# Kernel optimization log

Measured on AMD Instinct MI355X. Metric: run time of the kernel, lower is better.

## Reference

```python
import jax, jax.numpy as jnp
import numpy as np
import math

N_NODES = 50000
N_EDGES = 400000
D = 256
H = 4
HD = D // H


def _layernorm(x, g, b, eps=1e-5):
    mu = jnp.mean(x, axis=-1, keepdims=True)
    var = jnp.mean((x - mu) ** 2, axis=-1, keepdims=True)
    return (x - mu) * jax.lax.rsqrt(var + eps) * g + b


def setup_inputs() -> dict:
    key = jax.random.key(0)
    ks = jax.random.split(key, 16)
    init = lambda k, sh: (jax.random.normal(k, sh, dtype=jnp.float32) * 0.02)
    inp = {
        "h_n": jax.random.normal(ks[0], (N_NODES, D), dtype=jnp.float32),
        "h_e": jax.random.normal(ks[1], (N_EDGES, D), dtype=jnp.float32),
        "edge_index": jax.random.randint(ks[2], (2, N_EDGES), 0, N_NODES, dtype=jnp.int64),
        "Wq_w": init(ks[3], (2 * D, D)), "Wq_b": jnp.zeros((D,), jnp.float32),
        "Wkv_w": init(ks[4], (2 * D, 2 * D)), "Wkv_b": jnp.zeros((2 * D,), jnp.float32),
        "Wo_w": init(ks[5], (D, D)), "Wo_b": jnp.zeros((D,), jnp.float32),
        "ln1_g": jnp.ones((D,), jnp.float32), "ln1_b": jnp.zeros((D,), jnp.float32),
        "ffn1_w": init(ks[6], (D, 4 * D)), "ffn1_b": jnp.zeros((4 * D,), jnp.float32),
        "ffn2_w": init(ks[7], (4 * D, D)), "ffn2_b": jnp.zeros((D,), jnp.float32),
        "ln2_g": jnp.ones((D,), jnp.float32), "ln2_b": jnp.zeros((D,), jnp.float32),
    }
    return inp


def reference(h_n, h_e, edge_index, Wq_w, Wq_b, Wkv_w, Wkv_b, Wo_w, Wo_b,
              ln1_g, ln1_b, ffn1_w, ffn1_b, ffn2_w, ffn2_b, ln2_g, ln2_b):
    num_nodes = h_n.shape[0]
    src, dst = edge_index[0], edge_index[1]

    # edge gathers
    q_input = jnp.concatenate([h_n[src], h_e], axis=-1)   # (E, 2D)
    kv_input = jnp.concatenate([h_n[dst], h_e], axis=-1)  # (E, 2D)

    Q = q_input @ Wq_w + Wq_b                             # (E, D)
    KV = kv_input @ Wkv_w + Wkv_b                         # (E, 2D)
    K, V = KV[:, :D], KV[:, D:]

    Q = Q.reshape(-1, H, HD)
    K = K.reshape(-1, H, HD)
    V = V.reshape(-1, H, HD)

    scores = jnp.sum(Q * K, axis=-1) / math.sqrt(HD)      # (E, H)

    # scatter softmax over edges grouped by src node
    m = jax.ops.segment_max(scores, src, num_segments=num_nodes)  # (N, H)
    ex = jnp.exp(scores - m[src])
    denom = jax.ops.segment_sum(ex, src, num_segments=num_nodes)  # (N, H)
    attn = ex / denom[src]                                        # (E, H)

    # scatter-sum of weighted values back to src nodes
    wv = attn[:, :, None] * V                                     # (E, H, HD)
    out = jax.ops.segment_sum(wv, src, num_segments=num_nodes)    # (N, H, HD)
    out = out.reshape(num_nodes, D)
    out = out @ Wo_w + Wo_b

    h = _layernorm(h_n + out, ln1_g, ln1_b)
    ff = jax.nn.gelu(h @ ffn1_w + ffn1_b, approximate=False) @ ffn2_w + ffn2_b
    h = _layernorm(h + ff, ln2_g, ln2_b)
    return h
```

## Files before the change

kernel.cpp:

```cpp
#include <hip/hip_runtime.h>
#include <hip/hip_bf16.h>
#include <cstdint>
#include <cstddef>


typedef __bf16 bf16;
typedef bf16 bf16x8 __attribute__((ext_vector_type(8)));
typedef bf16 bf16x4v __attribute__((ext_vector_type(4)));
typedef float f32x4 __attribute__((ext_vector_type(4)));
typedef const uint32_t __attribute__((address_space(1)))* gas_u32p;
typedef uint32_t __attribute__((address_space(3)))* las_u32p;

#define DEV static __device__ __forceinline__

static constexpr int NN = 50000;
static constexpr int NE = 400000;

DEV void async_copy16(const void* g, void* l) {
  __builtin_amdgcn_global_load_lds((gas_u32p)g, (las_u32p)l, 16, 0, 0);
}
DEV float bf2f(bf16 x) { return (float)x; }
DEV bf16  f2bf(float x) { return (bf16)x; }

template <int KV>
__global__ __launch_bounds__(256, 2) void gemm_edge(
    const bf16* __restrict__ hn, const bf16* __restrict__ he,
    const int* __restrict__ idx, const bf16* __restrict__ WT,
    const float* __restrict__ bias, const bf16* __restrict__ Qbf,
    bf16* __restrict__ outbf, float* __restrict__ scores) {
  __shared__ bf16 Al[128 * 32];
  __shared__ bf16 Bl[128 * 32];
  const int tid = threadIdx.x;
  const int e0 = blockIdx.x * 128;
  const int n0 = blockIdx.y * 128;

  const bf16* an[2];
  const bf16* ae[2];
  const bf16* bb[2];
#pragma unroll
  for (int p = 0; p < 2; ++p) {
    int c = tid + 256 * p;
    int row = c >> 2;
    int c8 = (c & 3) * 8;
    int e = e0 + row;
    int node = idx[e];
    an[p] = hn + (size_t)node * 256 + c8;
    ae[p] = he + (size_t)e * 256 + c8;
    bb[p] = WT + (size_t)(n0 + row) * 512 + c8;
  }

  const int wv = tid >> 6, lane = tid & 63;
  const int quad = lane >> 4, l16 = lane & 15;
  const int wrow = (wv >> 1) * 64, wcol = (wv & 1) * 64;

  f32x4 acc[4][4] = {};

  for (int k0 = 0; k0 < 512; k0 += 32) {
    if (k0) __syncthreads();
#pragma unroll
    for (int p = 0; p < 2; ++p) {
      const bf16* ga = (k0 < 256) ? (an[p] + k0) : (ae[p] + (k0 - 256));
      async_copy16(ga, &Al[(tid + 256 * p) * 8]);
      async_copy16(bb[p] + k0, &Bl[(tid + 256 * p) * 8]);
    }
    __syncthreads();
    bf16x8 af[4], bfr[4];
#pragma unroll
    for (int t = 0; t < 4; ++t)
      af[t] = *(const bf16x8*)&Al[(wrow + t * 16 + l16) * 32 + quad * 8];
#pragma unroll
    for (int t = 0; t < 4; ++t)
      bfr[t] = *(const bf16x8*)&Bl[(wcol + t * 16 + l16) * 32 + quad * 8];
#pragma unroll
    for (int mt = 0; mt < 4; ++mt)
#pragma unroll
      for (int nt = 0; nt < 4; ++nt)
        acc[mt][nt] = __builtin_amdgcn_mfma_f32_16x16x32_bf16(
            af[mt], bfr[nt], acc[mt][nt], 0, 0, 0);
  }

  if (KV == 0) {
#pragma unroll
    for (int nt = 0; nt < 4; ++nt) {
      int col = n0 + wcol + nt * 16 + l16;
      float bv = bias[col];
#pragma unroll
      for (int mt = 0; mt < 4; ++mt)
#pragma unroll
        for (int r = 0; r < 4; ++r) {
          int row = e0 + wrow + mt * 16 + quad * 4 + r;
          outbf[(size_t)row * 256 + col] = f2bf(acc[mt][nt][r] + bv);
        }
    }
  } else if (blockIdx.y < 2) {
    const int head = (n0 + wcol) >> 6;
    float bv[4];
#pragma unroll
    for (int nt = 0; nt < 4; ++nt) bv[nt] = bias[n0 + wcol + nt * 16 + l16];
#pragma unroll
    for (int mt = 0; mt < 4; ++mt)
#pragma unroll
      for (int r = 0; r < 4; ++r) {
        int row = e0 + wrow + mt * 16 + quad * 4 + r;
        float part = 0.f;
#pragma unroll
        for (int nt = 0; nt < 4; ++nt) {
          int col = n0 + wcol + nt * 16 + l16;
          part += (acc[mt][nt][r] + bv[nt]) * bf2f(Qbf[(size_t)row * 256 + col]);
        }
        part += __shfl_xor(part, 1);
        part += __shfl_xor(part, 2);
        part += __shfl_xor(part, 4);
        part += __shfl_xor(part, 8);
        if (l16 == 0) scores[(size_t)row * 4 + head] = part * 0.125f;
      }
  } else {
#pragma unroll
    for (int nt = 0; nt < 4; ++nt) {
      int col = n0 + wcol + nt * 16 + l16;
      float bv = bias[col];
#pragma unroll
      for (int mt = 0; mt < 4; ++mt)
#pragma unroll
        for (int r = 0; r < 4; ++r) {
          int row = e0 + wrow + mt * 16 + quad * 4 + r;
          outbf[(size_t)row * 256 + (col - 256)] = f2bf(acc[mt][nt][r] + bv);
        }
    }
  }
}

template <int KT, int EPI>
__global__ __launch_bounds__(256, 2) void gemm_node(
    const bf16* __restrict__ A, int M, const bf16* __restrict__ WT,
    const float* __restrict__ bias, int Nout, float* __restrict__ outf,
    bf16* __restrict__ outb) {
  __shared__ bf16 Al[128 * 32];
  __shared__ bf16 Bl[128 * 32];
  const int tid = threadIdx.x;
  const int m0 = blockIdx.x * 128;
  const int n0 = blockIdx.y * 128;
  const bf16* ab[2];
  const bf16* bb[2];
#pragma unroll
  for (int p = 0; p < 2; ++p) {
    int c = tid + 256 * p;
    int row = c >> 2;
    int c8 = (c & 3) * 8;
    int rg = m0 + row;
    if (rg > M - 1) rg = M - 1;
    ab[p] = A + (size_t)rg * KT + c8;
    bb[p] = WT + (size_t)(n0 + row) * KT + c8;
  }
  const int wv = tid >> 6, lane = tid & 63;
  const int quad = lane >> 4, l16 = lane & 15;
  const int wrow = (wv >> 1) * 64, wcol = (wv & 1) * 64;
  f32x4 acc[4][4] = {};
  for (int k0 = 0; k0 < KT; k0 += 32) {
    if (k0) __syncthreads();
#pragma unroll
    for (int p = 0; p < 2; ++p) {
      async_copy16(ab[p] + k0, &Al[(tid + 256 * p) * 8]);
      async_copy16(bb[p] + k0, &Bl[(tid + 256 * p) * 8]);
    }
    __syncthreads();
    bf16x8 af[4], bfr[4];
#pragma unroll
    for (int t = 0; t < 4; ++t)
      af[t] = *(const bf16x8*)&Al[(wrow + t * 16 + l16) * 32 + quad * 8];
#pragma unroll
    for (int t = 0; t < 4; ++t)
      bfr[t] = *(const bf16x8*)&Bl[(wcol + t * 16 + l16) * 32 + quad * 8];
#pragma unroll
    for (int mt = 0; mt < 4; ++mt)
#pragma unroll
      for (int nt = 0; nt < 4; ++nt)
        acc[mt][nt] = __builtin_amdgcn_mfma_f32_16x16x32_bf16(
            af[mt], bfr[nt], acc[mt][nt], 0, 0, 0);
  }
#pragma unroll
  for (int nt = 0; nt < 4; ++nt) {
    int col = n0 + wcol + nt * 16 + l16;
    float bv = bias[col];
#pragma unroll
    for (int mt = 0; mt < 4; ++mt)
#pragma unroll
      for (int r = 0; r < 4; ++r) {
        int row = m0 + wrow + mt * 16 + quad * 4 + r;
        if (row < M) {
          float v = acc[mt][nt][r] + bv;
          if (EPI == 0)
            outf[(size_t)row * Nout + col] = v;
          else
            outb[(size_t)row * Nout + col] =
                f2bf(0.5f * v * (1.f + erff(v * 0.70710678118654752f)));
        }
      }
  }
}

__global__ __launch_bounds__(256) void cast_bf16(const float* __restrict__ in,
                                                 bf16* __restrict__ out, int n) {
  int i = (blockIdx.x * 256 + threadIdx.x) * 4;
  if (i < n) {
    float4 v = *(const float4*)(in + i);
    bf16x4v o = {f2bf(v.x), f2bf(v.y), f2bf(v.z), f2bf(v.w)};
    *(bf16x4v*)(out + i) = o;
  }
}

__global__ __launch_bounds__(256) void transpose_cast(
    const float* __restrict__ W, bf16* __restrict__ WT, int K, int N) {
  int i = blockIdx.x * 256 + threadIdx.x;
  if (i < K * N) {
    int k = i / N, n = i - k * N;
    WT[(size_t)n * K + k] = f2bf(W[i]);
  }
}

__global__ __launch_bounds__(256) void count_deg(const int* __restrict__ src,
                                                 int* __restrict__ deg, int nE) {
  int e = blockIdx.x * 256 + threadIdx.x;
  if (e < nE) atomicAdd(&deg[src[e]], 1);
}

__global__ __launch_bounds__(256) void scan_offs(const int* __restrict__ deg,
                                                 int* __restrict__ offs,
                                                 int* __restrict__ cursor,
                                                 int nN) {
  __shared__ int part[256];
  int tid = threadIdx.x;
  int per = (nN + 255) >> 8;
  int lo = tid * per, hi = lo + per;
  if (hi > nN) hi = nN;
  int sm = 0;
  for (int i = lo; i < hi; ++i) sm += deg[i];
  part[tid] = sm;
  __syncthreads();
  if (tid == 0) {
    int run = 0;
    for (int i = 0; i < 256; ++i) {
      int v = part[i];
      part[i] = run;
      run += v;
    }
  }
  __syncthreads();
  int run = part[tid];
  for (int i = lo; i < hi; ++i) {
    offs[i] = run;
    cursor[i] = run;
    run += deg[i];
  }
  if (tid == 255) offs[nN] = run;
}

__global__ __launch_bounds__(256) void scatter_edges(const int* __restrict__ src,
                                                     int* __restrict__ cursor,
                                                     int* __restrict__ eperm,
                                                     int nE) {
  int e = blockIdx.x * 256 + threadIdx.x;
  if (e < nE) {
    int p = atomicAdd(&cursor[src[e]], 1);
    eperm[p] = e;
  }
}

__global__ __launch_bounds__(256) void aggregate(
    const int* __restrict__ offs, const int* __restrict__ eperm,
    const float* __restrict__ scores, const bf16* __restrict__ Vbf,
    bf16* __restrict__ outbf) {
  int n = blockIdx.x;
  int s = offs[n];
  int deg = offs[n + 1] - s;
  int tid = threadIdx.x, wv = tid >> 6, lane = tid & 63;
  __shared__ float mdl[4], dnl[4];
  float mx = -3.4e38f;
  for (int i = lane; i < deg; i += 64) {
    int e = eperm[s + i];
    mx = fmaxf(mx, scores[(size_t)e * 4 + wv]);
  }
#pragma unroll
  for (int o = 32; o; o >>= 1) mx = fmaxf(mx, __shfl_xor(mx, o));
  float sm = 0.f;
  for (int i = lane; i < deg; i += 64) {
    int e = eperm[s + i];
    sm += expf(scores[(size_t)e * 4 + wv] - mx);
  }
#pragma unroll
  for (int o = 32; o; o >>= 1) sm += __shfl_xor(sm, o);
  if (lane == 0) {
    mdl[wv] = mx;
    dnl[wv] = sm;
  }
  __syncthreads();
  int c = tid, h = tid >> 6;
  float m = mdl[h];
  float rd = dnl[h] > 0.f ? 1.f / dnl[h] : 0.f;
  float acc = 0.f;
  for (int i = 0; i < deg; ++i) {
    int e = eperm[s + i];
    float w = expf(scores[(size_t)e * 4 + h] - m) * rd;
    acc += w * bf2f(Vbf[(size_t)e * 256 + c]);
  }
  outbf[(size_t)n * 256 + c] = f2bf(acc);
}

__global__ __launch_bounds__(256) void ln_kernel(
    const float* __restrict__ x1, const float* __restrict__ x2,
    const float* __restrict__ g, const float* __restrict__ b,
    float* __restrict__ outf, bf16* __restrict__ outb) {
  int n = blockIdx.x, tid = threadIdx.x;
  float x = x1[(size_t)n * 256 + tid] + x2[(size_t)n * 256 + tid];
  float s = x, s2 = x * x;
#pragma unroll
  for (int o = 32; o; o >>= 1) {
    s += __shfl_xor(s, o);
    s2 += __shfl_xor(s2, o);
  }
  __shared__ float ls[4], ls2[4];
  int wv = tid >> 6, lane = tid & 63;
  if (lane == 0) {
    ls[wv] = s;
    ls2[wv] = s2;
  }
  __syncthreads();
  s = ls[0] + ls[1] + ls[2] + ls[3];
  s2 = ls2[0] + ls2[1] + ls2[2] + ls2[3];
  float mu = s * (1.f / 256.f);
  float var = s2 * (1.f / 256.f) - mu * mu;
  float y = (x - mu) * rsqrtf(var + 1e-5f) * g[tid] + b[tid];
  if (outf) outf[(size_t)n * 256 + tid] = y;
  if (outb) outb[(size_t)n * 256 + tid] = f2bf(y);
}

static constexpr size_t OFF_HN = 0;
static constexpr size_t OFF_HE = OFF_HN + 25600000;
static constexpr size_t OFF_WQT = OFF_HE + 204800000;
static constexpr size_t OFF_WKVT = OFF_WQT + 262144;
static constexpr size_t OFF_WOT = OFF_WKVT + 524288;
static constexpr size_t OFF_W1T = OFF_WOT + 131072;
static constexpr size_t OFF_W2T = OFF_W1T + 524288;
static constexpr size_t OFF_SC = OFF_W2T + 524288;
static constexpr size_t OFF_DEG = OFF_SC + 6400000;
static constexpr size_t OFF_OFFS = OFF_DEG + 200000;
static constexpr size_t OFF_CUR = OFF_OFFS + 200064;
static constexpr size_t OFF_EPERM = OFF_CUR + 200000;
static constexpr size_t OFF_AOUT = OFF_EPERM + 1600000;
static constexpr size_t OFF_Q = OFF_AOUT + 25600000;
static constexpr size_t OFF_V = OFF_Q + 204800000;
static constexpr size_t OFF_TMP = OFF_Q;
static constexpr size_t OFF_H1F = OFF_Q + 51200000;
static constexpr size_t OFF_H1B = OFF_Q + 102400000;
static constexpr size_t OFF_TMP2 = OFF_Q + 128000000;
static constexpr size_t OFF_FFM = OFF_HE;

extern "C" void kernel_launch(void* const* d_in, const int* in_sizes, int n_in,
                              void* d_out, int out_size, void* d_ws,
                              size_t ws_size, hipStream_t stream) {
  const float* h_n = (const float*)d_in[0];
  const float* h_e = (const float*)d_in[1];
  const int* eidx = (const int*)d_in[2];
  const int* src = eidx;
  const int* dst = eidx + NE;
  const float* Wq_w = (const float*)d_in[3];
  const float* Wq_b = (const float*)d_in[4];
  const float* Wkv_w = (const float*)d_in[5];
  const float* Wkv_b = (const float*)d_in[6];
  const float* Wo_w = (const float*)d_in[7];
  const float* Wo_b = (const float*)d_in[8];
  const float* ln1_g = (const float*)d_in[9];
  const float* ln1_b = (const float*)d_in[10];
  const float* f1_w = (const float*)d_in[11];
  const float* f1_b = (const float*)d_in[12];
  const float* f2_w = (const float*)d_in[13];
  const float* f2_b = (const float*)d_in[14];
  const float* ln2_g = (const float*)d_in[15];
  const float* ln2_b = (const float*)d_in[16];

  uint8_t* ws = (uint8_t*)d_ws;
  bf16* hn_bf = (bf16*)(ws + OFF_HN);
  bf16* he_bf = (bf16*)(ws + OFF_HE);
  bf16* WqT = (bf16*)(ws + OFF_WQT);
  bf16* WkvT = (bf16*)(ws + OFF_WKVT);
  bf16* WoT = (bf16*)(ws + OFF_WOT);
  bf16* W1T = (bf16*)(ws + OFF_W1T);
  bf16* W2T = (bf16*)(ws + OFF_W2T);
  float* scores = (float*)(ws + OFF_SC);
  int* deg = (int*)(ws + OFF_DEG);
  int* offs = (int*)(ws + OFF_OFFS);
  int* cursor = (int*)(ws + OFF_CUR);
  int* eperm = (int*)(ws + OFF_EPERM);
  bf16* aout = (bf16*)(ws + OFF_AOUT);
  bf16* Qbf = (bf16*)(ws + OFF_Q);
  bf16* Vbf = (bf16*)(ws + OFF_V);
  float* tmp = (float*)(ws + OFF_TMP);
  float* h1f = (float*)(ws + OFF_H1F);
  bf16* h1b = (bf16*)(ws + OFF_H1B);
  float* tmp2 = (float*)(ws + OFF_TMP2);
  bf16* ffm = (bf16*)(ws + OFF_FFM);

  cast_bf16<<<12500, 256, 0, stream>>>(h_n, hn_bf, NN * 256);
  cast_bf16<<<100000, 256, 0, stream>>>(h_e, he_bf, NE * 256);
  transpose_cast<<<512, 256, 0, stream>>>(Wq_w, WqT, 512, 256);
  transpose_cast<<<1024, 256, 0, stream>>>(Wkv_w, WkvT, 512, 512);
  transpose_cast<<<256, 256, 0, stream>>>(Wo_w, WoT, 256, 256);
  transpose_cast<<<1024, 256, 0, stream>>>(f1_w, W1T, 256, 1024);
  transpose_cast<<<1024, 256, 0, stream>>>(f2_w, W2T, 1024, 256);

  hipMemsetAsync(deg, 0, NN * sizeof(int), stream);
  count_deg<<<1563, 256, 0, stream>>>(src, deg, NE);
  scan_offs<<<1, 256, 0, stream>>>(deg, offs, cursor, NN);
  scatter_edges<<<1563, 256, 0, stream>>>(src, cursor, eperm, NE);

  gemm_edge<0><<<dim3(3125, 2), 256, 0, stream>>>(hn_bf, he_bf, src, WqT, Wq_b,
                                                  nullptr, Qbf, nullptr);
  gemm_edge<1><<<dim3(3125, 4), 256, 0, stream>>>(hn_bf, he_bf, dst, WkvT,
                                                  Wkv_b, Qbf, Vbf, scores);

  aggregate<<<NN, 256, 0, stream>>>(offs, eperm, scores, Vbf, aout);

  gemm_node<256, 0><<<dim3(391, 2), 256, 0, stream>>>(aout, NN, WoT, Wo_b, 256,
                                                      tmp, nullptr);
  ln_kernel<<<NN, 256, 0, stream>>>(h_n, tmp, ln1_g, ln1_b, h1f, h1b);

  gemm_node<256, 1><<<dim3(391, 8), 256, 0, stream>>>(h1b, NN, W1T, f1_b, 1024,
                                                      nullptr, ffm);
  gemm_node<1024, 0><<<dim3(391, 2), 256, 0, stream>>>(ffm, NN, W2T, f2_b, 256,
                                                       tmp2, nullptr);
  ln_kernel<<<NN, 256, 0, stream>>>(h1f, tmp2, ln2_g, ln2_b, (float*)d_out,
                                    nullptr);
}
```

Baseline: 1.893 ms.

## Split node/edge projections and fold V projection into output weight

Uses linearity to project node features once per node (50k rows) instead of per gathered edge, and adds the gathered node projection in the edge GEMM epilogues. The V projection is eliminated by aggregating raw hn[dst] and he rows per head and multiplying by a precomputed Wkv_V·Wo combined weight (K=2048) at node level. This cuts edge-level GEMM FLOPs and V writes, but adds fp32 node-projection gathers, a per-head 2048-wide aggregated buffer, and a larger node GEMM. Grid axes are also swapped so N-tiles vary fastest.

```diff
diff --git a/kernel.cpp b/kernel.cpp
--- a/kernel.cpp
+++ b/kernel.cpp
@@ -21,114 +21,6 @@
 }
 DEV float bf2f(bf16 x) { return (float)x; }
 DEV bf16  f2bf(float x) { return (bf16)x; }
-
-template <int KV>
-__global__ __launch_bounds__(256, 2) void gemm_edge(
-    const bf16* __restrict__ hn, const bf16* __restrict__ he,
-    const int* __restrict__ idx, const bf16* __restrict__ WT,
-    const float* __restrict__ bias, const bf16* __restrict__ Qbf,
-    bf16* __restrict__ outbf, float* __restrict__ scores) {
-  __shared__ bf16 Al[128 * 32];
-  __shared__ bf16 Bl[128 * 32];
-  const int tid = threadIdx.x;
-  const int e0 = blockIdx.x * 128;
-  const int n0 = blockIdx.y * 128;
-
-  const bf16* an[2];
-  const bf16* ae[2];
-  const bf16* bb[2];
-#pragma unroll
-  for (int p = 0; p < 2; ++p) {
-    int c = tid + 256 * p;
-    int row = c >> 2;
-    int c8 = (c & 3) * 8;
-    int e = e0 + row;
-    int node = idx[e];
-    an[p] = hn + (size_t)node * 256 + c8;
-    ae[p] = he + (size_t)e * 256 + c8;
-    bb[p] = WT + (size_t)(n0 + row) * 512 + c8;
-  }
-
-  const int wv = tid >> 6, lane = tid & 63;
-  const int quad = lane >> 4, l16 = lane & 15;
-  const int wrow = (wv >> 1) * 64, wcol = (wv & 1) * 64;
-
-  f32x4 acc[4][4] = {};
-
-  for (int k0 = 0; k0 < 512; k0 += 32) {
-    if (k0) __syncthreads();
-#pragma unroll
-    for (int p = 0; p < 2; ++p) {
-      const bf16* ga = (k0 < 256) ? (an[p] + k0) : (ae[p] + (k0 - 256));
-      async_copy16(ga, &Al[(tid + 256 * p) * 8]);
-      async_copy16(bb[p] + k0, &Bl[(tid + 256 * p) * 8]);
-    }
-    __syncthreads();
-    bf16x8 af[4], bfr[4];
-#pragma unroll
-    for (int t = 0; t < 4; ++t)
-      af[t] = *(const bf16x8*)&Al[(wrow + t * 16 + l16) * 32 + quad * 8];
-#pragma unroll
-    for (int t = 0; t < 4; ++t)
-      bfr[t] = *(const bf16x8*)&Bl[(wcol + t * 16 + l16) * 32 + quad * 8];
-#pragma unroll
-    for (int mt = 0; mt < 4; ++mt)
-#pragma unroll
-      for (int nt = 0; nt < 4; ++nt)
-        acc[mt][nt] = __builtin_amdgcn_mfma_f32_16x16x32_bf16(
-            af[mt], bfr[nt], acc[mt][nt], 0, 0, 0);
-  }
-
-  if (KV == 0) {
-#pragma unroll
-    for (int nt = 0; nt < 4; ++nt) {
-      int col = n0 + wcol + nt * 16 + l16;
-      float bv = bias[col];
-#pragma unroll
-      for (int mt = 0; mt < 4; ++mt)
-#pragma unroll
-        for (int r = 0; r < 4; ++r) {
-          int row = e0 + wrow + mt * 16 + quad * 4 + r;
-          outbf[(size_t)row * 256 + col] = f2bf(acc[mt][nt][r] + bv);
-        }
-    }
-  } else if (blockIdx.y < 2) {
-    const int head = (n0 + wcol) >> 6;
-    float bv[4];
-#pragma unroll
-    for (int nt = 0; nt < 4; ++nt) bv[nt] = bias[n0 + wcol + nt * 16 + l16];
-#pragma unroll
-    for (int mt = 0; mt < 4; ++mt)
-#pragma unroll
-      for (int r = 0; r < 4; ++r) {
-        int row = e0 + wrow + mt * 16 + quad * 4 + r;
-        float part = 0.f;
-#pragma unroll
-        for (int nt = 0; nt < 4; ++nt) {
-          int col = n0 + wcol + nt * 16 + l16;
-          part += (acc[mt][nt][r] + bv[nt]) * bf2f(Qbf[(size_t)row * 256 + col]);
-        }
-        part += __shfl_xor(part, 1);
-        part += __shfl_xor(part, 2);
-        part += __shfl_xor(part, 4);
-        part += __shfl_xor(part, 8);
-        if (l16 == 0) scores[(size_t)row * 4 + head] = part * 0.125f;
-      }
-  } else {
-#pragma unroll
-    for (int nt = 0; nt < 4; ++nt) {
-      int col = n0 + wcol + nt * 16 + l16;
-      float bv = bias[col];
-#pragma unroll
-      for (int mt = 0; mt < 4; ++mt)
-#pragma unroll
-        for (int r = 0; r < 4; ++r) {
-          int row = e0 + wrow + mt * 16 + quad * 4 + r;
-          outbf[(size_t)row * 256 + (col - 256)] = f2bf(acc[mt][nt][r] + bv);
-        }
-    }
-  }
-}
 
 template <int KT, int EPI>
 __global__ __launch_bounds__(256, 2) void gemm_node(
@@ -138,8 +30,8 @@
   __shared__ bf16 Al[128 * 32];
   __shared__ bf16 Bl[128 * 32];
   const int tid = threadIdx.x;
-  const int m0 = blockIdx.x * 128;
-  const int n0 = blockIdx.y * 128;
+  const int n0 = blockIdx.x * 128;
+  const int m0 = blockIdx.y * 128;
   const bf16* ab[2];
   const bf16* bb[2];
 #pragma unroll
@@ -181,7 +73,7 @@
 #pragma unroll
   for (int nt = 0; nt < 4; ++nt) {
     int col = n0 + wcol + nt * 16 + l16;
-    float bv = bias[col];
+    float bv = bias ? bias[col] : 0.f;
 #pragma unroll
     for (int mt = 0; mt < 4; ++mt)
 #pragma unroll
@@ -191,12 +83,150 @@
           float v = acc[mt][nt][r] + bv;
           if (EPI == 0)
             outf[(size_t)row * Nout + col] = v;
-          else
+          else if (EPI == 1)
             outb[(size_t)row * Nout + col] =
                 f2bf(0.5f * v * (1.f + erff(v * 0.70710678118654752f)));
+          else
+            outb[(size_t)row * Nout + col] = f2bf(v);
         }
       }
   }
+}
+
+__global__ __launch_bounds__(256, 2) void gemm_eeq(
+    const bf16* __restrict__ he, const bf16* __restrict__ WT,
+    const float* __restrict__ bias, const int* __restrict__ src,
+    const float* __restrict__ ENf, bf16* __restrict__ Qout) {
+  __shared__ bf16 Al[128 * 32];
+  __shared__ bf16 Bl[128 * 32];
+  const int tid = threadIdx.x;
+  const int n0 = blockIdx.x * 128;
+  const int m0 = blockIdx.y * 128;
+  const bf16* ab[2];
+  const bf16* bb[2];
+#pragma unroll
+  for (int p = 0; p < 2; ++p) {
+    int c = tid + 256 * p;
+    int row = c >> 2;
+    int c8 = (c & 3) * 8;
+    ab[p] = he + (size_t)(m0 + row) * 256 + c8;
+    bb[p] = WT + (size_t)(n0 + row) * 256 + c8;
+  }
+  const int wv = tid >> 6, lane = tid & 63;
+  const int quad = lane >> 4, l16 = lane & 15;
+  const int wrow = (wv >> 1) * 64, wcol = (wv & 1) * 64;
+  f32x4 acc[4][4] = {};
+  for (int k0 = 0; k0 < 256; k0 += 32) {
+    if (k0) __syncthreads();
+#pragma unroll
+    for (int p = 0; p < 2; ++p) {
+      async_copy16(ab[p] + k0, &Al[(tid + 256 * p) * 8]);
+      async_copy16(bb[p] + k0, &Bl[(tid + 256 * p) * 8]);
+    }
+    __syncthreads();
+    bf16x8 af[4], bfr[4];
+#pragma unroll
+    for (int t = 0; t < 4; ++t)
+      af[t] = *(const bf16x8*)&Al[(wrow + t * 16 + l16) * 32 + quad * 8];
+#pragma unroll
+    for (int t = 0; t < 4; ++t)
+      bfr[t] = *(const bf16x8*)&Bl[(wcol + t * 16 + l16) * 32 + quad * 8];
+#pragma unroll
+    for (int mt = 0; mt < 4; ++mt)
+#pragma unroll
+      for (int nt = 0; nt < 4; ++nt)
+        acc[mt][nt] = __builtin_amdgcn_mfma_f32_16x16x32_bf16(
+            af[mt], bfr[nt], acc[mt][nt], 0, 0, 0);
+  }
+  float bv[4];
+#pragma unroll
+  for (int nt = 0; nt < 4; ++nt) bv[nt] = bias[n0 + wcol + nt * 16 + l16];
+#pragma unroll
+  for (int mt = 0; mt < 4; ++mt)
+#pragma unroll
+    for (int r = 0; r < 4; ++r) {
+      int row = m0 + wrow + mt * 16 + quad * 4 + r;
+      int s = src[row];
+      const float* en = ENf + (size_t)s * 512;
+#pragma unroll
+      for (int nt = 0; nt < 4; ++nt) {
+        int col = n0 + wcol + nt * 16 + l16;
+        Qout[(size_t)row * 256 + col] = f2bf(acc[mt][nt][r] + bv[nt] + en[col]);
+      }
+    }
+}
+
+__global__ __launch_bounds__(256, 2) void gemm_eek(
+    const bf16* __restrict__ he, const bf16* __restrict__ WT,
+    const float* __restrict__ bias, const int* __restrict__ dstp,
+    const float* __restrict__ ENf, const bf16* __restrict__ Qbf,
+    float* __restrict__ scores) {
+  __shared__ bf16 Al[128 * 32];
+  __shared__ bf16 Bl[128 * 32];
+  const int tid = threadIdx.x;
+  const int n0 = blockIdx.x * 128;
+  const int m0 = blockIdx.y * 128;
+  const bf16* ab[2];
+  const bf16* bb[2];
+#pragma unroll
+  for (int p = 0; p < 2; ++p) {
+    int c = tid + 256 * p;
+    int row = c >> 2;
+    int c8 = (c & 3) * 8;
+    ab[p] = he + (size_t)(m0 + row) * 256 + c8;
+    bb[p] = WT + (size_t)(n0 + row) * 256 + c8;
+  }
+  const int wv = tid >> 6, lane = tid & 63;
+  const int quad = lane >> 4, l16 = lane & 15;
+  const int wrow = (wv >> 1) * 64, wcol = (wv & 1) * 64;
+  f32x4 acc[4][4] = {};
+  for (int k0 = 0; k0 < 256; k0 += 32) {
+    if (k0) __syncthreads();
+#pragma unroll
+    for (int p = 0; p < 2; ++p) {
+      async_copy16(ab[p] + k0, &Al[(tid + 256 * p) * 8]);
+      async_copy16(bb[p] + k0, &Bl[(tid + 256 * p) * 8]);
+    }
+    __syncthreads();
+    bf16x8 af[4], bfr[4];
+#pragma unroll
+    for (int t = 0; t < 4; ++t)
+      af[t] = *(const bf16x8*)&Al[(wrow + t * 16 + l16) * 32 + quad * 8];
+#pragma unroll
+    for (int t = 0; t < 4; ++t)
+      bfr[t] = *(const bf16x8*)&Bl[(wcol + t * 16 + l16) * 32 + quad * 8];
+#pragma unroll
+    for (int mt = 0; mt < 4; ++mt)
+#pragma unroll
+      for (int nt = 0; nt < 4; ++nt)
+        acc[mt][nt] = __builtin_amdgcn_mfma_f32_16x16x32_bf16(
+            af[mt], bfr[nt], acc[mt][nt], 0, 0, 0);
+  }
+  float bv[4];
+#pragma unroll
+  for (int nt = 0; nt < 4; ++nt) bv[nt] = bias[n0 + wcol + nt * 16 + l16];
+  const int head = (n0 + wcol) >> 6;
+#pragma unroll
+  for (int mt = 0; mt < 4; ++mt)
+#pragma unroll
+    for (int r = 0; r < 4; ++r) {
+      int row = m0 + wrow + mt * 16 + quad * 4 + r;
+      int d = dstp[row];
+      const float* en = ENf + (size_t)d * 512 + 256;
+      const bf16* qr = Qbf + (size_t)row * 256;
+      float part = 0.f;
+#pragma unroll
+      for (int nt = 0; nt < 4; ++nt) {
+        int col = n0 + wcol + nt * 16 + l16;
+        float kv = acc[mt][nt][r] + bv[nt] + en[col];
+        part += kv * bf2f(qr[col]);
+      }
+      part += __shfl_xor(part, 1);
+      part += __shfl_xor(part, 2);
+      part += __shfl_xor(part, 4);
+      part += __shfl_xor(part, 8);
+      if (l16 == 0) scores[(size_t)row * 4 + head] = part * 0.125f;
+    }
 }
 
 __global__ __launch_bounds__(256) void cast_bf16(const float* __restrict__ in,
@@ -216,6 +246,51 @@
     int k = i / N, n = i - k * N;
     WT[(size_t)n * K + k] = f2bf(W[i]);
   }
+}
+
+__global__ __launch_bounds__(256) void build_wnet(
+    const float* __restrict__ Wq, const float* __restrict__ Wkv,
+    bf16* __restrict__ WnT, bf16* __restrict__ WeT) {
+  int n = blockIdx.x, k = threadIdx.x;
+  float vn, ve;
+  if (n < 256) {
+    vn = Wq[(size_t)k * 256 + n];
+    ve = Wq[(size_t)(256 + k) * 256 + n];
+  } else {
+    vn = Wkv[(size_t)k * 512 + (n - 256)];
+    ve = Wkv[(size_t)(256 + k) * 512 + (n - 256)];
+  }
+  WnT[(size_t)n * 256 + k] = f2bf(vn);
+  WeT[(size_t)n * 256 + k] = f2bf(ve);
+}
+
+__global__ __launch_bounds__(256) void build_wcomb(
+    const float* __restrict__ Wkv, const float* __restrict__ Wkv_b,
+    const float* __restrict__ Wo, const float* __restrict__ Wo_b,
+    bf16* __restrict__ WcombT, float* __restrict__ bias_vo) {
+  int j = blockIdx.x, t = threadIdx.x;
+  __shared__ float wo[256];
+  wo[t] = Wo[(size_t)t * 256 + j];
+  __syncthreads();
+#pragma unroll
+  for (int p = 0; p < 8; ++p) {
+    int idx = p * 256 + t;
+    int h = idx >> 9, i = idx & 511;
+    const float* wrow = Wkv + (size_t)i * 512 + 256 + h * 64;
+    const float* wob = wo + h * 64;
+    float s = 0.f;
+#pragma unroll 8
+    for (int m = 0; m < 64; ++m) s += wrow[m] * wob[m];
+    WcombT[(size_t)j * 2048 + idx] = f2bf(s);
+  }
+  float bs = Wkv_b[256 + t] * wo[t];
+#pragma unroll
+  for (int o = 32; o; o >>= 1) bs += __shfl_xor(bs, o);
+  __shared__ float red[4];
+  int wv = t >> 6, lane = t & 63;
+  if (lane == 0) red[wv] = bs;
+  __syncthreads();
+  if (t == 0) bias_vo[j] = red[0] + red[1] + red[2] + red[3] + Wo_b[j];
 }
 
 __global__ __launch_bounds__(256) void count_deg(const int* __restrict__ src,
@@ -268,8 +343,9 @@
 
 __global__ __launch_bounds__(256) void aggregate(
     const int* __restrict__ offs, const int* __restrict__ eperm,
-    const float* __restrict__ scores, const bf16* __restrict__ Vbf,
-    bf16* __restrict__ outbf) {
+    const int* __restrict__ dstp, const float* __restrict__ scores,
+    const bf16* __restrict__ hn, const bf16* __restrict__ he,
+    bf16* __restrict__ aggH) {
   int n = blockIdx.x;
   int s = offs[n];
   int deg = offs[n + 1] - s;
@@ -294,16 +370,34 @@
     dnl[wv] = sm;
   }
   __syncthreads();
-  int c = tid, h = tid >> 6;
-  float m = mdl[h];
-  float rd = dnl[h] > 0.f ? 1.f / dnl[h] : 0.f;
-  float acc = 0.f;
+  float m[4], rd[4];
+#pragma unroll
+  for (int h = 0; h < 4; ++h) {
+    m[h] = mdl[h];
+    rd[h] = dnl[h] > 0.f ? 1.f / dnl[h] : 0.f;
+  }
+  float accn[4] = {}, acce[4] = {};
   for (int i = 0; i < deg; ++i) {
     int e = eperm[s + i];
-    float w = expf(scores[(size_t)e * 4 + h] - m) * rd;
-    acc += w * bf2f(Vbf[(size_t)e * 256 + c]);
-  }
-  outbf[(size_t)n * 256 + c] = f2bf(acc);
+    int d = dstp[e];
+    f32x4 sc = *(const f32x4*)(scores + (size_t)e * 4);
+    float w[4];
+#pragma unroll
+    for (int h = 0; h < 4; ++h) w[h] = expf(sc[h] - m[h]) * rd[h];
+    float xn = bf2f(hn[(size_t)d * 256 + tid]);
+    float xe = bf2f(he[(size_t)e * 256 + tid]);
+#pragma unroll
+    for (int h = 0; h < 4; ++h) {
+      accn[h] += w[h] * xn;
+      acce[h] += w[h] * xe;
+    }
+  }
+  bf16* out = aggH + (size_t)n * 2048;
+#pragma unroll
+  for (int h = 0; h < 4; ++h) {
+    out[h * 512 + tid] = f2bf(accn[h]);
+    out[h * 512 + 256 + tid] = f2bf(acce[h]);
+  }
 }
 
 __global__ __launch_bounds__(256) void ln_kernel(
@@ -334,26 +428,27 @@
   if (outb) outb[(size_t)n * 256 + tid] = f2bf(y);
 }
 
-static constexpr size_t OFF_HN = 0;
-static constexpr size_t OFF_HE = OFF_HN + 25600000;
-static constexpr size_t OFF_WQT = OFF_HE + 204800000;
-static constexpr size_t OFF_WKVT = OFF_WQT + 262144;
-static constexpr size_t OFF_WOT = OFF_WKVT + 524288;
-static constexpr size_t OFF_W1T = OFF_WOT + 131072;
-static constexpr size_t OFF_W2T = OFF_W1T + 524288;
-static constexpr size_t OFF_SC = OFF_W2T + 524288;
-static constexpr size_t OFF_DEG = OFF_SC + 6400000;
-static constexpr size_t OFF_OFFS = OFF_DEG + 200000;
-static constexpr size_t OFF_CUR = OFF_OFFS + 200064;
-static constexpr size_t OFF_EPERM = OFF_CUR + 200000;
-static constexpr size_t OFF_AOUT = OFF_EPERM + 1600000;
-static constexpr size_t OFF_Q = OFF_AOUT + 25600000;
-static constexpr size_t OFF_V = OFF_Q + 204800000;
-static constexpr size_t OFF_TMP = OFF_Q;
-static constexpr size_t OFF_H1F = OFF_Q + 51200000;
-static constexpr size_t OFF_H1B = OFF_Q + 102400000;
-static constexpr size_t OFF_TMP2 = OFF_Q + 128000000;
-static constexpr size_t OFF_FFM = OFF_HE;
+static constexpr size_t OFF_HN    = 0;
+static constexpr size_t OFF_HE    = 25600000;
+static constexpr size_t OFF_WNT   = 230400000;
+static constexpr size_t OFF_WET   = 230662144;
+static constexpr size_t OFF_WCT   = 230924288;
+static constexpr size_t OFF_W1T   = 231972864;
+static constexpr size_t OFF_W2T   = 232497152;
+static constexpr size_t OFF_BVO   = 233021440;
+static constexpr size_t OFF_SC    = 233022464;
+static constexpr size_t OFF_DEG   = 239422464;
+static constexpr size_t OFF_OFFS  = 239622464;
+static constexpr size_t OFF_CUR   = 239822528;
+static constexpr size_t OFF_EPERM = 240022528;
+static constexpr size_t OFF_ENF   = 241622528;
+static constexpr size_t OFF_Q     = 344022528;
+static constexpr size_t OFF_AGGH  = OFF_Q;
+static constexpr size_t OFF_TMP   = OFF_HE;
+static constexpr size_t OFF_H1F   = OFF_HE + 51200000;
+static constexpr size_t OFF_H1B   = OFF_HE + 102400000;
+static constexpr size_t OFF_TMP2  = OFF_HE + 128000000;
+static constexpr size_t OFF_FFM   = OFF_Q;
 
 extern "C" void kernel_launch(void* const* d_in, const int* in_sizes, int n_in,
                               void* d_out, int out_size, void* d_ws,
@@ -381,19 +476,20 @@
   uint8_t* ws = (uint8_t*)d_ws;
   bf16* hn_bf = (bf16*)(ws + OFF_HN);
   bf16* he_bf = (bf16*)(ws + OFF_HE);
-  bf16* WqT = (bf16*)(ws + OFF_WQT);
-  bf16* WkvT = (bf16*)(ws + OFF_WKVT);
-  bf16* WoT = (bf16*)(ws + OFF_WOT);
+  bf16* WnT = (bf16*)(ws + OFF_WNT);
+  bf16* WeT = (bf16*)(ws + OFF_WET);
+  bf16* WcombT = (bf16*)(ws + OFF_WCT);
   bf16* W1T = (bf16*)(ws + OFF_W1T);
   bf16* W2T = (bf16*)(ws + OFF_W2T);
+  float* bias_vo = (float*)(ws + OFF_BVO);
   float* scores = (float*)(ws + OFF_SC);
   int* deg = (int*)(ws + OFF_DEG);
   int* offs = (int*)(ws + OFF_OFFS);
   int* cursor = (int*)(ws + OFF_CUR);
   int* eperm = (int*)(ws + OFF_EPERM);
-  bf16* aout = (bf16*)(ws + OFF_AOUT);
+  float* ENf = (float*)(ws + OFF_ENF);
   bf16* Qbf = (bf16*)(ws + OFF_Q);
-  bf16* Vbf = (bf16*)(ws + OFF_V);
+  bf16* aggH = (bf16*)(ws + OFF_AGGH);
   float* tmp = (float*)(ws + OFF_TMP);
   float* h1f = (float*)(ws + OFF_H1F);
   bf16* h1b = (bf16*)(ws + OFF_H1B);
@@ -402,9 +498,9 @@
 
   cast_bf16<<<12500, 256, 0, stream>>>(h_n, hn_bf, NN * 256);
   cast_bf16<<<100000, 256, 0, stream>>>(h_e, he_bf, NE * 256);
-  transpose_cast<<<512, 256, 0, stream>>>(Wq_w, WqT, 512, 256);
-  transpose_cast<<<1024, 256, 0, stream>>>(Wkv_w, WkvT, 512, 512);
-  transpose_cast<<<256, 256, 0, stream>>>(Wo_w, WoT, 256, 256);
+  build_wnet<<<512, 256, 0, stream>>>(Wq_w, Wkv_w, WnT, WeT);
+  build_wcomb<<<256, 256, 0, stream>>>(Wkv_w, Wkv_b, Wo_w, Wo_b, WcombT,
+                                       bias_vo);
   transpose_cast<<<1024, 256, 0, stream>>>(f1_w, W1T, 256, 1024);
   transpose_cast<<<1024, 256, 0, stream>>>(f2_w, W2T, 1024, 256);
 
@@ -413,20 +509,23 @@
   scan_offs<<<1, 256, 0, stream>>>(deg, offs, cursor, NN);
   scatter_edges<<<1563, 256, 0, stream>>>(src, cursor, eperm, NE);
 
-  gemm_edge<0><<<dim3(3125, 2), 256, 0, stream>>>(hn_bf, he_bf, src, WqT, Wq_b,
-                                                  nullptr, Qbf, nullptr);
-  gemm_edge<1><<<dim3(3125, 4), 256, 0, stream>>>(hn_bf, he_bf, dst, WkvT,
-                                                  Wkv_b, Qbf, Vbf, scores);
-
-  aggregate<<<NN, 256, 0, stream>>>(offs, eperm, scores, Vbf, aout);
-
-  gemm_node<256, 0><<<dim3(391, 2), 256, 0, stream>>>(aout, NN, WoT, Wo_b, 256,
-                                                      tmp, nullptr);
+  gemm_node<256, 0><<<dim3(4, 391), 256, 0, stream>>>(hn_bf, NN, WnT, nullptr,
+                                                      512, ENf, nullptr);
+  gemm_eeq<<<dim3(2, 3125), 256, 0, stream>>>(he_bf, WeT, Wq_b, src, ENf, Qbf);
+  gemm_eek<<<dim3(2, 3125), 256, 0, stream>>>(he_bf, WeT + 256 * 256, Wkv_b,
+                                              dst, ENf, Qbf, scores);
+
+  aggregate<<<NN, 256, 0, stream>>>(offs, eperm, dst, scores, hn_bf, he_bf,
+                                    aggH);
+
+  gemm_node<2048, 0><<<dim3(2, 391), 256, 0, stream>>>(aggH, NN, WcombT,
+                                                       bias_vo, 256, tmp,
+                                                       nullptr);
   ln_kernel<<<NN, 256, 0, stream>>>(h_n, tmp, ln1_g, ln1_b, h1f, h1b);
 
-  gemm_node<256, 1><<<dim3(391, 8), 256, 0, stream>>>(h1b, NN, W1T, f1_b, 1024,
+  gemm_node<256, 1><<<dim3(8, 391), 256, 0, stream>>>(h1b, NN, W1T, f1_b, 1024,
                                                       nullptr, ffm);
-  gemm_node<1024, 0><<<dim3(391, 2), 256, 0, stream>>>(ffm, NN, W2T, f2_b, 256,
+  gemm_node<1024, 0><<<dim3(2, 391), 256, 0, stream>>>(ffm, NN, W2T, f2_b, 256,
                                                        tmp2, nullptr);
   ln_kernel<<<NN, 256, 0, stream>>>(h1f, tmp2, ln2_g, ln2_b, (float*)d_out,
                                     nullptr);
```

Result: no change. 1.896 ms (+0.2%).
